# Performance work log

Measured on AMD Instinct MI355X. Metric: run time of the kernel, lower is better.

Reference implementation:

```python
import jax, jax.numpy as jnp
import numpy as np

NUM_ITER = 20
EPS = 1e-8


def _conv(x, w, pad):
    # x: [N, Cin, H, W], w: [Cout, Cin, kh, kw] (cross-correlation, like torch conv2d)
    return jax.lax.conv_general_dilated(
        x, w, window_strides=(1, 1), padding=pad,
        dimension_numbers=('NCHW', 'OIHW', 'NCHW'))


def setup_inputs() -> dict:
    key = jax.random.key(0)
    x = jax.random.normal(key, (2, 4, 3, 256, 256), dtype=jnp.float32)
    return {
        'x': x,
        'lam': jnp.array([0.02], dtype=jnp.float32),
        'tau': jnp.array([0.25], dtype=jnp.float32),
        'theta': jnp.array([0.1], dtype=jnp.float32),
        'wx': jnp.array([[-1.0, 1.0, 0.0]], dtype=jnp.float32),
        'wy': jnp.array([[-1.0], [1.0], [0.0]], dtype=jnp.float32),
    }


def reference(x, lam, tau, theta, wx, wy):
    # x: [2, B, C, H, W] -> pairs of single-channel images [NB, 2, H, W]
    F, B, C, H, W = x.shape
    NB = B * C
    xx = jnp.moveaxis(x.reshape(2, NB, H, W), 0, 1)  # [NB, 2, H, W]

    dt = x.dtype
    gx = jnp.array([[-1., 0., 1.], [-2., 0., 2.], [-1., 0., 1.]], dt) / 6.0
    gy = jnp.array([[-1., -2., -1.], [0., 0., 0.], [1., 2., 1.]], dt) / 6.0
    grad_w = jnp.stack([gx, gy])[:, None]          # [2,1,3,3] image gradient (fixed)
    gxu = jnp.array([[0., 0., 0.], [0., -1., 1.], [0., 0., 0.]], dt)
    gyu = jnp.array([[0., 0., 0.], [0., -1., 0.], [0., 1., 0.]], dt)
    grad_u_w = jnp.stack([gxu, gyu])[:, None]      # [2,1,3,3] flow gradient (fixed)
    wx_k = wx[None, None]                          # [1,1,1,3] trainable divergence stencil
    wy_k = wy[None, None]                          # [1,1,3,1]

    rho_c = (xx[:, 1] - xx[:, 0])[:, None]                       # [NB,1,H,W]
    grad_im = _conv(xx[:, 1:], grad_w, [(1, 1), (1, 1)])         # [NB,2,H,W]
    norm_grad = jnp.sum(grad_im * grad_im, axis=1, keepdims=True) + EPS

    u = jnp.zeros((NB, 2, H, W), dt)
    p1 = jnp.zeros((NB, 2, H, W), dt)
    p2 = jnp.zeros((NB, 2, H, W), dt)

    tl = theta * lam       # [1]
    tt = tau / theta       # [1]

    def div(p):  # p: [NB,2,H,W] -> [NB,1,H,W]
        return (_conv(p[:, 0:1], wx_k, [(0, 0), (1, 1)]) +
                _conv(p[:, 1:2], wy_k, [(1, 1), (0, 0)]))

    def body(carry, _):
        u, p1, p2 = carry
        rho = rho_c + jnp.sum(grad_im * u, axis=1, keepdims=True)
        th = tl * norm_grad
        v = u - jnp.where(jnp.abs(rho) < th,
                          rho * grad_im / norm_grad,
                          tl * grad_im * jnp.sign(rho))
        u0 = v[:, 0] + theta * div(p1)[:, 0]
        u1 = v[:, 1] + theta * div(p2)[:, 0]
        u = jnp.stack([u0, u1], axis=1)
        g1 = _conv(u[:, 0:1], grad_u_w, [(1, 1), (1, 1)])
        g2 = _conv(u[:, 1:2], grad_u_w, [(1, 1), (1, 1)])
        p1 = (p1 + tt * g1) / (1.0 + tt * jnp.sum(jnp.abs(g1), axis=1, keepdims=True))
        p2 = (p2 + tt * g2) / (1.0 + tt * jnp.sum(jnp.abs(g2), axis=1, keepdims=True))
        return (u, p1, p2), None

    (u, p1, p2), _ = jax.lax.scan(body, (u, p1, p2), None, length=NUM_ITER)
    return u.reshape(B, C, 2, H, W)
```

## Files before the change

kernel.cpp:

```cpp
#include <hip/hip_runtime.h>

#define W 256
#define H 256
#define HW (W*H)
#define NB 12
#define ROWS 16
#define BPI (H/ROWS)
#define NBLK (NB*BPI)
#define NTHREADS 1024
#define NUM_ITER 20
#define TVEPS 1e-8f
#define HPLANES 6
#define FLAG_MAGIC 0x5A170000


__device__ __forceinline__ float aload(const float* p) {
    return __hip_atomic_load(p, __ATOMIC_RELAXED, __HIP_MEMORY_SCOPE_AGENT);
}
__device__ __forceinline__ void astore(float* p, float v) {
    __hip_atomic_store(p, v, __ATOMIC_RELAXED, __HIP_MEMORY_SCOPE_AGENT);
}
__device__ __forceinline__ void waitflag(const int* f, int tgt) {
    while (__hip_atomic_load(f, __ATOMIC_RELAXED, __HIP_MEMORY_SCOPE_AGENT) != tgt)
        __builtin_amdgcn_s_sleep(1);
    asm volatile("" ::: "memory");
}
__device__ __forceinline__ void setflag(int* f, int tgt) {
    asm volatile("s_waitcnt vmcnt(0)" ::: "memory");
    __hip_atomic_store(f, tgt, __ATOMIC_RELAXED, __HIP_MEMORY_SCOPE_AGENT);
}
__device__ __forceinline__ float fastrcp(float x) { return __builtin_amdgcn_rcpf(x); }

#define LD4(dst, ptr) { const float4 _t = *reinterpret_cast<const float4*>(ptr); \
                        dst[0]=_t.x; dst[1]=_t.y; dst[2]=_t.z; dst[3]=_t.w; }
#define ST4(ptr, src) { float4 _t; _t.x=src[0]; _t.y=src[1]; _t.z=src[2]; _t.w=src[3]; \
                        *reinterpret_cast<float4*>(ptr) = _t; }

__global__ __launch_bounds__(NTHREADS, 1) void tvl1_uex_kernel(
    const float* __restrict__ xin,
    const float* __restrict__ lam,
    const float* __restrict__ tau,
    const float* __restrict__ theta,
    const float* __restrict__ wxv,
    const float* __restrict__ wyv,
    float* __restrict__ uout,
    float* __restrict__ halo,
    int* __restrict__ flags)
{
    __shared__ float xu0[ROWS][W];
    __shared__ float xu1[ROWS][W];
    __shared__ float xq1[ROWS][W];
    __shared__ float xq2[ROWS][W];

    const int tid  = threadIdx.x;
    const int lane = tid & 63;
    const int wv   = tid >> 6;
    const int x0   = lane << 2;
    const int b    = blockIdx.x;
    const int n    = b / BPI, bi = b % BPI;
    const int r0   = bi * ROWS;
    const int grow = r0 + wv;
    const bool notTop = (bi > 0), notBot = (bi < BPI-1);

    const float th0 = theta[0];
    const float tl  = th0 * lam[0];
    const float tt  = tau[0] / th0;
    const float wx0 = wxv[0], wx1 = wxv[1], wx2 = wxv[2];
    const float wy0 = wyv[0], wy1 = wyv[1], wy2 = wyv[2];

    const float* __restrict__ I0 = xin + (size_t)n * HW;
    const float* __restrict__ I1 = xin + (size_t)(NB + n) * HW;

    float rho[4], gxr[4], gyr[4];
    {
        #pragma unroll
        for (int c = 0; c < 4; ++c) {
            const int xc = x0 + c;
            const int idx = grow * W + xc;
            const bool xm = xc > 0, xp = xc < W-1, ym = grow > 0, yp = grow < H-1;
            float a00=0.f,a01=0.f,a02=0.f,a10=0.f,a12=0.f,a20=0.f,a21=0.f,a22=0.f;
            if (ym) { a01=I1[idx-W]; if (xm) a00=I1[idx-W-1]; if (xp) a02=I1[idx-W+1]; }
            if (xm) a10=I1[idx-1];
            if (xp) a12=I1[idx+1];
            if (yp) { a21=I1[idx+W]; if (xm) a20=I1[idx+W-1]; if (xp) a22=I1[idx+W+1]; }
            gxr[c] = ((a02-a00) + 2.f*(a12-a10) + (a22-a20)) * (1.f/6.f);
            gyr[c] = ((a20-a00) + 2.f*(a21-a01) + (a22-a02)) * (1.f/6.f);
            rho[c] = I1[idx] - I0[idx];
        }
    }

    for (int k = tid; k < ROWS*W; k += NTHREADS) {
        (&xu0[0][0])[k]=0.f; (&xu1[0][0])[k]=0.f;
        (&xq1[0][0])[k]=0.f; (&xq2[0][0])[k]=0.f;
    }
    float u0[4]={0,0,0,0}, u1[4]={0,0,0,0};
    float p1x[4]={0,0,0,0}, p1y[4]={0,0,0,0}, p2x[4]={0,0,0,0}, p2y[4]={0,0,0,0};
    __syncthreads();

    for (int it = 0; it < NUM_ITER; ++it) {
        const bool last = (it == NUM_ITER-1);

        float hym1[4]={0,0,0,0}, hym2[4]={0,0,0,0};
        float hyp1[4]={0,0,0,0}, hyp2[4]={0,0,0,0};
        if (it > 0) {
            int* fb = flags + (size_t)(it-1) * 3 * NBLK;
            const int tgt = FLAG_MAGIC | (it-1);
            if (wv == 0 && notTop) {
                if (lane == 0) waitflag(&fb[1*NBLK + (b-1)], tgt);
                const float* hu = halo + ((size_t)(it-1)*NBLK + (b-1)) * HPLANES * W;
                #pragma unroll
                for (int c = 0; c < 4; ++c) {
                    hym1[c] = aload(hu + 2*W + x0 + c);
                    hym2[c] = aload(hu + 3*W + x0 + c);
                }
            }
            if (wv == 15 && notBot) {
                if (lane == 0) waitflag(&fb[0*NBLK + (b+1)], tgt);
                const float* hd = halo + ((size_t)(it-1)*NBLK + (b+1)) * HPLANES * W;
                #pragma unroll
                for (int c = 0; c < 4; ++c) {
                    hyp1[c] = aload(hd + 0*W + x0 + c);
                    hyp2[c] = aload(hd + 1*W + x0 + c);
                }
            }
        }

        float pym1[4], pym2[4], pyp1[4], pyp2[4];
        if (wv > 0) { LD4(pym1, &xq1[wv-1][x0]); LD4(pym2, &xq2[wv-1][x0]); }
        else        { for (int c=0;c<4;++c){ pym1[c]=hym1[c]; pym2[c]=hym2[c]; } }
        if (wv < ROWS-1) { LD4(pyp1, &xq1[wv+1][x0]); LD4(pyp2, &xq2[wv+1][x0]); }
        else             { for (int c=0;c<4;++c){ pyp1[c]=hyp1[c]; pyp2[c]=hyp2[c]; } }

        float l1 = __shfl_up(p1x[3], 1);   float l2 = __shfl_up(p2x[3], 1);
        if (lane == 0) { l1 = 0.f; l2 = 0.f; }
        float r1 = __shfl_down(p1x[0], 1); float r2 = __shfl_down(p2x[0], 1);
        if (lane == 63) { r1 = 0.f; r2 = 0.f; }
        const float p1xm[4] = { l1, p1x[0], p1x[1], p1x[2] };
        const float p1xp[4] = { p1x[1], p1x[2], p1x[3], r1 };
        const float p2xm[4] = { l2, p2x[0], p2x[1], p2x[2] };
        const float p2xp[4] = { p2x[1], p2x[2], p2x[3], r2 };

        #pragma unroll
        for (int c = 0; c < 4; ++c) {
            const float r  = rho[c] + gxr[c]*u0[c] + gyr[c]*u1[c];
            const float ng = gxr[c]*gxr[c] + gyr[c]*gyr[c] + TVEPS;
            const float th = tl * ng;
            const float f  = (fabsf(r) < th) ? (r * fastrcp(ng)) : copysignf(tl, r);
            const float d1 = wx0*p1xm[c] + wx1*p1x[c] + wx2*p1xp[c]
                           + wy0*pym1[c] + wy1*p1y[c] + wy2*pyp1[c];
            const float d2 = wx0*p2xm[c] + wx1*p2x[c] + wx2*p2xp[c]
                           + wy0*pym2[c] + wy1*p2y[c] + wy2*pyp2[c];
            u0[c] = (u0[c] - f*gxr[c]) + th0*d1;
            u1[c] = (u1[c] - f*gyr[c]) + th0*d2;
        }

        if (last) {
            float* __restrict__ o0 = uout + (size_t)(2*n)   * HW + (size_t)grow * W + x0;
            float* __restrict__ o1 = uout + (size_t)(2*n+1) * HW + (size_t)grow * W + x0;
            ST4(o0, u0); ST4(o1, u1);
            break;
        }

        float* hwp = halo + ((size_t)it * NBLK + b) * HPLANES * W;
        int* fw = flags + (size_t)it * 3 * NBLK;
        const int ftgt = FLAG_MAGIC | it;
        if (wv == 0 && notTop) {
            #pragma unroll
            for (int c = 0; c < 4; ++c) {
                astore(hwp + 4*W + x0 + c, u0[c]);
                astore(hwp + 5*W + x0 + c, u1[c]);
            }
            if (lane == 0) setflag(&fw[2*NBLK + b], ftgt);
        }
        ST4(&xu0[wv][x0], u0); ST4(&xu1[wv][x0], u1);
        __syncthreads();

        float uy0[4], uy1[4];
        if (wv < ROWS-1) { LD4(uy0, &xu0[wv+1][x0]); LD4(uy1, &xu1[wv+1][x0]); }
        else if (grow == H-1) { for (int c=0;c<4;++c){ uy0[c]=0.f; uy1[c]=0.f; } }
        else {
            if (lane == 0) waitflag(&fw[2*NBLK + (b+1)], ftgt);
            const float* hd = halo + ((size_t)it*NBLK + (b+1)) * HPLANES * W;
            #pragma unroll
            for (int c = 0; c < 4; ++c) {
                uy0[c] = aload(hd + 4*W + x0 + c);
                uy1[c] = aload(hd + 5*W + x0 + c);
            }
        }
        float ur0 = __shfl_down(u0[0], 1), ur1 = __shfl_down(u1[0], 1);
        if (lane == 63) { ur0 = 0.f; ur1 = 0.f; }
        #pragma unroll
        for (int c = 0; c < 4; ++c) {
            const float uxp0 = (c < 3) ? u0[c+1] : ur0;
            const float uxp1 = (c < 3) ? u1[c+1] : ur1;
            const float g1x = uxp0 - u0[c];
            const float g1y = uy0[c] - u0[c];
            const float g2x = uxp1 - u1[c];
            const float g2y = uy1[c] - u1[c];
            const float rc1 = fastrcp(1.f + tt * (fabsf(g1x) + fabsf(g1y)));
            const float rc2 = fastrcp(1.f + tt * (fabsf(g2x) + fabsf(g2y)));
            p1x[c] = (p1x[c] + tt*g1x) * rc1;
            p1y[c] = (p1y[c] + tt*g1y) * rc1;
            p2x[c] = (p2x[c] + tt*g2x) * rc2;
            p2y[c] = (p2y[c] + tt*g2y) * rc2;
        }
        ST4(&xq1[wv][x0], p1y); ST4(&xq2[wv][x0], p2y);

        if (wv == 0 && notTop) {
            #pragma unroll
            for (int c = 0; c < 4; ++c) {
                astore(hwp + 0*W + x0 + c, p1y[c]);
                astore(hwp + 1*W + x0 + c, p2y[c]);
            }
            if (lane == 0) setflag(&fw[0*NBLK + b], ftgt);
        } else if (wv == ROWS-1 && notBot) {
            #pragma unroll
            for (int c = 0; c < 4; ++c) {
                astore(hwp + 2*W + x0 + c, p1y[c]);
                astore(hwp + 3*W + x0 + c, p2y[c]);
            }
            if (lane == 0) setflag(&fw[1*NBLK + b], ftgt);
        }
        __syncthreads();
    }
}


__global__ void precompute_kernel(const float* __restrict__ x,
                                  float* __restrict__ u,
                                  float* __restrict__ ws) {
    const int row = blockIdx.x;
    const int n = row / H, y = row % H;
    const int xx = threadIdx.x;
    const int idx = y * W + xx;
    const float* __restrict__ I0 = x + (size_t)n * HW;
    const float* __restrict__ I1 = x + (size_t)(NB + n) * HW;
    float* __restrict__ p1  = ws;
    float* __restrict__ p2  = ws + (size_t)2 * NB * HW;
    float* __restrict__ rho = ws + (size_t)4 * NB * HW;
    float* __restrict__ gxp = ws + (size_t)5 * NB * HW;
    float* __restrict__ gyp = ws + (size_t)6 * NB * HW;
    const float i1c = I1[idx];
    const bool xm = xx > 0, xp = xx < W - 1, ym = y > 0, yp = y < H - 1;
    float a00=0.f,a01=0.f,a02=0.f,a10=0.f,a12=0.f,a20=0.f,a21=0.f,a22=0.f;
    if (ym) { a01 = I1[idx-W]; if (xm) a00 = I1[idx-W-1]; if (xp) a02 = I1[idx-W+1]; }
    if (xm) a10 = I1[idx-1];
    if (xp) a12 = I1[idx+1];
    if (yp) { a21 = I1[idx+W]; if (xm) a20 = I1[idx+W-1]; if (xp) a22 = I1[idx+W+1]; }
    const float gxv = ((a02-a00) + 2.f*(a12-a10) + (a22-a20)) * (1.f/6.f);
    const float gyv = ((a20-a00) + 2.f*(a21-a01) + (a22-a02)) * (1.f/6.f);
    const size_t np = (size_t)n * HW;
    rho[np+idx] = i1c - I0[idx];
    gxp[np+idx] = gxv;
    gyp[np+idx] = gyv;
    u[(size_t)(2*n)*HW + idx] = 0.f;   u[(size_t)(2*n+1)*HW + idx] = 0.f;
    p1[(size_t)(2*n)*HW + idx] = 0.f;  p1[(size_t)(2*n+1)*HW + idx] = 0.f;
    p2[(size_t)(2*n)*HW + idx] = 0.f;  p2[(size_t)(2*n+1)*HW + idx] = 0.f;
}

__global__ void u_kernel(const float* __restrict__ ws,
                         float* __restrict__ u,
                         const float* __restrict__ lam,
                         const float* __restrict__ theta,
                         const float* __restrict__ wxv,
                         const float* __restrict__ wyv) {
    const int row = blockIdx.x;
    const int n = row / H, y = row % H;
    const int xx = threadIdx.x;
    const int idx = y * W + xx;
    const size_t np = (size_t)n * HW;
    const float* __restrict__ p1  = ws;
    const float* __restrict__ p2  = ws + (size_t)2 * NB * HW;
    const float* __restrict__ rho_c = ws + (size_t)4 * NB * HW;
    const float* __restrict__ gxp = ws + (size_t)5 * NB * HW;
    const float* __restrict__ gyp = ws + (size_t)6 * NB * HW;
    const float th0 = theta[0];
    const float tl = th0 * lam[0];
    const float wx0 = wxv[0], wx1 = wxv[1], wx2 = wxv[2];
    const float wy0 = wyv[0], wy1 = wyv[1], wy2 = wyv[2];
    const float gx = gxp[np+idx];
    const float gy = gyp[np+idx];
    float* __restrict__ u0p = u + (size_t)(2*n)*HW;
    float* __restrict__ u1p = u + (size_t)(2*n+1)*HW;
    const float u0 = u0p[idx], u1 = u1p[idx];
    const float rho = rho_c[np+idx] + gx*u0 + gy*u1;
    const float ng = gx*gx + gy*gy + TVEPS;
    const float th = tl * ng;
    float s0, s1;
    if (fabsf(rho) < th) { const float d = rho/ng; s0 = d*gx; s1 = d*gy; }
    else { const float sg = (rho > 0.f) ? 1.f : ((rho < 0.f) ? -1.f : 0.f);
           s0 = tl*gx*sg; s1 = tl*gy*sg; }
    const float v0 = u0 - s0, v1 = u1 - s1;
    const float* __restrict__ p1x = p1 + (size_t)(2*n)*HW;
    const float* __restrict__ p1y = p1 + (size_t)(2*n+1)*HW;
    const float* __restrict__ p2x = p2 + (size_t)(2*n)*HW;
    const float* __restrict__ p2y = p2 + (size_t)(2*n+1)*HW;
    float d1 = wx1*p1x[idx] + wy1*p1y[idx];
    float d2 = wx1*p2x[idx] + wy1*p2y[idx];
    if (xx > 0)     { d1 += wx0*p1x[idx-1]; d2 += wx0*p2x[idx-1]; }
    if (xx < W-1)   { d1 += wx2*p1x[idx+1]; d2 += wx2*p2x[idx+1]; }
    if (y > 0)      { d1 += wy0*p1y[idx-W]; d2 += wy0*p2y[idx-W]; }
    if (y < H-1)    { d1 += wy2*p1y[idx+W]; d2 += wy2*p2y[idx+W]; }
    u0p[idx] = v0 + th0*d1;
    u1p[idx] = v1 + th0*d2;
}

__global__ void p_kernel(const float* __restrict__ u,
                         float* __restrict__ ws,
                         const float* __restrict__ tau,
                         const float* __restrict__ theta) {
    const int row = blockIdx.x;
    const int n = row / H, y = row % H;
    const int xx = threadIdx.x;
    const int idx = y * W + xx;
    float* __restrict__ p1 = ws;
    float* __restrict__ p2 = ws + (size_t)2 * NB * HW;
    const float tt = tau[0] / theta[0];
    const float* __restrict__ u0p = u + (size_t)(2*n)*HW;
    const float* __restrict__ u1p = u + (size_t)(2*n+1)*HW;
    const float c0 = u0p[idx];
    const float g1x = ((xx < W-1) ? u0p[idx+1] : 0.f) - c0;
    const float g1y = ((y < H-1) ? u0p[idx+W] : 0.f) - c0;
    const float c1 = u1p[idx];
    const float g2x = ((xx < W-1) ? u1p[idx+1] : 0.f) - c1;
    const float g2y = ((y < H-1) ? u1p[idx+W] : 0.f) - c1;
    float* __restrict__ p1x = p1 + (size_t)(2*n)*HW;
    float* __restrict__ p1y = p1 + (size_t)(2*n+1)*HW;
    float* __restrict__ p2x = p2 + (size_t)(2*n)*HW;
    float* __restrict__ p2y = p2 + (size_t)(2*n+1)*HW;
    const float den1 = 1.f + tt * (fabsf(g1x) + fabsf(g1y));
    p1x[idx] = (p1x[idx] + tt*g1x) / den1;
    p1y[idx] = (p1y[idx] + tt*g1y) / den1;
    const float den2 = 1.f + tt * (fabsf(g2x) + fabsf(g2y));
    p2x[idx] = (p2x[idx] + tt*g2x) / den2;
    p2y[idx] = (p2y[idx] + tt*g2y) / den2;
}

extern "C" void kernel_launch(void* const* d_in, const int* in_sizes, int n_in,
                              void* d_out, int out_size, void* d_ws, size_t ws_size,
                              hipStream_t stream) {
    const float* x     = (const float*)d_in[0];
    const float* lam   = (const float*)d_in[1];
    const float* tau   = (const float*)d_in[2];
    const float* theta = (const float*)d_in[3];
    const float* wxv   = (const float*)d_in[4];
    const float* wyv   = (const float*)d_in[5];
    float* u = (float*)d_out;

    const size_t halo_floats = (size_t)(NUM_ITER-1) * NBLK * HPLANES * W;
    const size_t need = halo_floats * sizeof(float)
                      + (size_t)(NUM_ITER-1) * 3 * NBLK * sizeof(int);

    if (ws_size >= need) {
        float* halo = (float*)d_ws;
        int* flags = (int*)((char*)d_ws + halo_floats * sizeof(float));
        void* args[] = { (void*)&x, (void*)&lam, (void*)&tau, (void*)&theta,
                         (void*)&wxv, (void*)&wyv, (void*)&u, (void*)&halo, (void*)&flags };
        hipLaunchCooperativeKernel((void*)tvl1_uex_kernel, dim3(NBLK), dim3(NTHREADS),
                                   args, 0, stream);
    } else {
        float* ws = (float*)d_ws;
        const dim3 grid(NB * H);
        const dim3 block(W);
        precompute_kernel<<<grid, block, 0, stream>>>(x, u, ws);
        for (int it = 0; it < NUM_ITER; ++it) {
            u_kernel<<<grid, block, 0, stream>>>(ws, u, lam, theta, wxv, wyv);
            p_kernel<<<grid, block, 0, stream>>>(u, ws, tau, theta);
        }
    }
}
```

Baseline: 102.4 us.

## Recompute neighbor halo row locally to remove mid-iteration cross-block wait

Replaces the per-iteration exchange of u halo rows with redundant recomputation: the bottom wave computes the u update for the next block's first row itself, using p values that neighbor publishes in the previous iteration. Edge waves also compute their u update before waiting on halo flags and add the halo contribution afterward, so the flag wait overlaps with compute. This removes one inter-block flag wait per iteration at the cost of extra halo planes, extra global stores and loads, and duplicated arithmetic on one wave.

```diff
diff --git a/kernel.cpp b/kernel.cpp
--- a/kernel.cpp
+++ b/kernel.cpp
@@ -10,7 +10,7 @@
 #define NTHREADS 1024
 #define NUM_ITER 20
 #define TVEPS 1e-8f
-#define HPLANES 6
+#define HPLANES 8
 #define FLAG_MAGIC 0x5A170000
 
 
@@ -35,8 +35,9 @@
                         dst[0]=_t.x; dst[1]=_t.y; dst[2]=_t.z; dst[3]=_t.w; }
 #define ST4(ptr, src) { float4 _t; _t.x=src[0]; _t.y=src[1]; _t.z=src[2]; _t.w=src[3]; \
                         *reinterpret_cast<float4*>(ptr) = _t; }
-
-__global__ __launch_bounds__(NTHREADS, 1) void tvl1_uex_kernel(
+#define CP4(dst, src) { _Pragma("unroll") for (int c = 0; c < 4; ++c) dst[c] = src[c]; }
+
+__global__ __launch_bounds__(NTHREADS, 1) void tvl1_dfr_kernel(
     const float* __restrict__ xin,
     const float* __restrict__ lam,
     const float* __restrict__ tau,
@@ -71,23 +72,28 @@
     const float* __restrict__ I0 = xin + (size_t)n * HW;
     const float* __restrict__ I1 = xin + (size_t)(NB + n) * HW;
 
-    float rho[4], gxr[4], gyr[4];
-    {
+    auto grad4 = [&](int row, float* rr, float* ggx, float* ggy) {
         #pragma unroll
         for (int c = 0; c < 4; ++c) {
             const int xc = x0 + c;
-            const int idx = grow * W + xc;
-            const bool xm = xc > 0, xp = xc < W-1, ym = grow > 0, yp = grow < H-1;
+            const int idx = row * W + xc;
+            const bool xm = xc > 0, xp = xc < W-1, ym = row > 0, yp = row < H-1;
             float a00=0.f,a01=0.f,a02=0.f,a10=0.f,a12=0.f,a20=0.f,a21=0.f,a22=0.f;
             if (ym) { a01=I1[idx-W]; if (xm) a00=I1[idx-W-1]; if (xp) a02=I1[idx-W+1]; }
             if (xm) a10=I1[idx-1];
             if (xp) a12=I1[idx+1];
             if (yp) { a21=I1[idx+W]; if (xm) a20=I1[idx+W-1]; if (xp) a22=I1[idx+W+1]; }
-            gxr[c] = ((a02-a00) + 2.f*(a12-a10) + (a22-a20)) * (1.f/6.f);
-            gyr[c] = ((a20-a00) + 2.f*(a21-a01) + (a22-a02)) * (1.f/6.f);
-            rho[c] = I1[idx] - I0[idx];
-        }
-    }
+            ggx[c] = ((a02-a00) + 2.f*(a12-a10) + (a22-a20)) * (1.f/6.f);
+            ggy[c] = ((a20-a00) + 2.f*(a21-a01) + (a22-a02)) * (1.f/6.f);
+            rr[c]  = I1[idx] - I0[idx];
+        }
+    };
+
+    float rho[4], gxr[4], gyr[4];
+    grad4(grow, rho, gxr, gyr);
+    float rho16[4]={0,0,0,0}, gx16[4]={0,0,0,0}, gy16[4]={0,0,0,0};
+    float u16_0[4]={0,0,0,0}, u16_1[4]={0,0,0,0};
+    if (wv == 15 && notBot) grad4(r0 + ROWS, rho16, gx16, gy16);
 
     for (int k = tid; k < ROWS*W; k += NTHREADS) {
         (&xu0[0][0])[k]=0.f; (&xu1[0][0])[k]=0.f;
@@ -97,61 +103,147 @@
     float p1x[4]={0,0,0,0}, p1y[4]={0,0,0,0}, p2x[4]={0,0,0,0}, p2y[4]={0,0,0,0};
     __syncthreads();
 
-    for (int it = 0; it < NUM_ITER; ++it) {
-        const bool last = (it == NUM_ITER-1);
-
-        float hym1[4]={0,0,0,0}, hym2[4]={0,0,0,0};
-        float hyp1[4]={0,0,0,0}, hyp2[4]={0,0,0,0};
-        if (it > 0) {
-            int* fb = flags + (size_t)(it-1) * 3 * NBLK;
-            const int tgt = FLAG_MAGIC | (it-1);
-            if (wv == 0 && notTop) {
-                if (lane == 0) waitflag(&fb[1*NBLK + (b-1)], tgt);
-                const float* hu = halo + ((size_t)(it-1)*NBLK + (b-1)) * HPLANES * W;
-                #pragma unroll
-                for (int c = 0; c < 4; ++c) {
-                    hym1[c] = aload(hu + 2*W + x0 + c);
-                    hym2[c] = aload(hu + 3*W + x0 + c);
-                }
-            }
-            if (wv == 15 && notBot) {
-                if (lane == 0) waitflag(&fb[0*NBLK + (b+1)], tgt);
-                const float* hd = halo + ((size_t)(it-1)*NBLK + (b+1)) * HPLANES * W;
-                #pragma unroll
-                for (int c = 0; c < 4; ++c) {
-                    hyp1[c] = aload(hd + 0*W + x0 + c);
-                    hyp2[c] = aload(hd + 1*W + x0 + c);
-                }
-            }
-        }
-
-        float pym1[4], pym2[4], pyp1[4], pyp2[4];
-        if (wv > 0) { LD4(pym1, &xq1[wv-1][x0]); LD4(pym2, &xq2[wv-1][x0]); }
-        else        { for (int c=0;c<4;++c){ pym1[c]=hym1[c]; pym2[c]=hym2[c]; } }
-        if (wv < ROWS-1) { LD4(pyp1, &xq1[wv+1][x0]); LD4(pyp2, &xq2[wv+1][x0]); }
-        else             { for (int c=0;c<4;++c){ pyp1[c]=hyp1[c]; pyp2[c]=hyp2[c]; } }
-
-        float l1 = __shfl_up(p1x[3], 1);   float l2 = __shfl_up(p2x[3], 1);
+    auto ustep_dym = [&](const float* rr, const float* ggx, const float* ggy,
+                         const float* uu0, const float* uu1,
+                         const float* x1, const float* q1c, const float* q1p,
+                         const float* x2, const float* q2c, const float* q2p,
+                         float* o0, float* o1) {
+        float l1 = __shfl_up(x1[3],1), l2 = __shfl_up(x2[3],1);
         if (lane == 0) { l1 = 0.f; l2 = 0.f; }
-        float r1 = __shfl_down(p1x[0], 1); float r2 = __shfl_down(p2x[0], 1);
+        float r1 = __shfl_down(x1[0],1), r2 = __shfl_down(x2[0],1);
         if (lane == 63) { r1 = 0.f; r2 = 0.f; }
-        const float p1xm[4] = { l1, p1x[0], p1x[1], p1x[2] };
-        const float p1xp[4] = { p1x[1], p1x[2], p1x[3], r1 };
-        const float p2xm[4] = { l2, p2x[0], p2x[1], p2x[2] };
-        const float p2xp[4] = { p2x[1], p2x[2], p2x[3], r2 };
-
+        const float x1m[4]={l1,x1[0],x1[1],x1[2]}, x1p[4]={x1[1],x1[2],x1[3],r1};
+        const float x2m[4]={l2,x2[0],x2[1],x2[2]}, x2p[4]={x2[1],x2[2],x2[3],r2};
+        #pragma unroll
+        for (int c = 0; c < 4; ++c) {
+            const float r  = rr[c] + ggx[c]*uu0[c] + ggy[c]*uu1[c];
+            const float ng = ggx[c]*ggx[c] + ggy[c]*ggy[c] + TVEPS;
+            const float f  = (fabsf(r) < tl*ng) ? (r * fastrcp(ng)) : copysignf(tl, r);
+            const float d1 = wx0*x1m[c] + wx1*x1[c] + wx2*x1p[c] + wy1*q1c[c] + wy2*q1p[c];
+            const float d2 = wx0*x2m[c] + wx1*x2[c] + wx2*x2p[c] + wy1*q2c[c] + wy2*q2p[c];
+            o0[c] = (uu0[c] - f*ggx[c]) + th0*d1;
+            o1[c] = (uu1[c] - f*ggy[c]) + th0*d2;
+        }
+    };
+    auto ustep_dyp = [&](const float* rr, const float* ggx, const float* ggy,
+                         const float* uu0, const float* uu1,
+                         const float* x1, const float* q1m, const float* q1c,
+                         const float* x2, const float* q2m, const float* q2c,
+                         float* o0, float* o1) {
+        float l1 = __shfl_up(x1[3],1), l2 = __shfl_up(x2[3],1);
+        if (lane == 0) { l1 = 0.f; l2 = 0.f; }
+        float r1 = __shfl_down(x1[0],1), r2 = __shfl_down(x2[0],1);
+        if (lane == 63) { r1 = 0.f; r2 = 0.f; }
+        const float x1m[4]={l1,x1[0],x1[1],x1[2]}, x1p[4]={x1[1],x1[2],x1[3],r1};
+        const float x2m[4]={l2,x2[0],x2[1],x2[2]}, x2p[4]={x2[1],x2[2],x2[3],r2};
+        #pragma unroll
+        for (int c = 0; c < 4; ++c) {
+            const float r  = rr[c] + ggx[c]*uu0[c] + ggy[c]*uu1[c];
+            const float ng = ggx[c]*ggx[c] + ggy[c]*ggy[c] + TVEPS;
+            const float f  = (fabsf(r) < tl*ng) ? (r * fastrcp(ng)) : copysignf(tl, r);
+            const float d1 = wx0*x1m[c] + wx1*x1[c] + wx2*x1p[c] + wy0*q1m[c] + wy1*q1c[c];
+            const float d2 = wx0*x2m[c] + wx1*x2[c] + wx2*x2p[c] + wy0*q2m[c] + wy1*q2c[c];
+            o0[c] = (uu0[c] - f*ggx[c]) + th0*d1;
+            o1[c] = (uu1[c] - f*ggy[c]) + th0*d2;
+        }
+    };
+    auto ustepF = [&](const float* q1m, const float* q1p, const float* q2m, const float* q2p) {
+        float l1 = __shfl_up(p1x[3],1), l2 = __shfl_up(p2x[3],1);
+        if (lane == 0) { l1 = 0.f; l2 = 0.f; }
+        float r1 = __shfl_down(p1x[0],1), r2 = __shfl_down(p2x[0],1);
+        if (lane == 63) { r1 = 0.f; r2 = 0.f; }
+        const float x1m[4]={l1,p1x[0],p1x[1],p1x[2]}, x1p[4]={p1x[1],p1x[2],p1x[3],r1};
+        const float x2m[4]={l2,p2x[0],p2x[1],p2x[2]}, x2p[4]={p2x[1],p2x[2],p2x[3],r2};
         #pragma unroll
         for (int c = 0; c < 4; ++c) {
             const float r  = rho[c] + gxr[c]*u0[c] + gyr[c]*u1[c];
             const float ng = gxr[c]*gxr[c] + gyr[c]*gyr[c] + TVEPS;
-            const float th = tl * ng;
-            const float f  = (fabsf(r) < th) ? (r * fastrcp(ng)) : copysignf(tl, r);
-            const float d1 = wx0*p1xm[c] + wx1*p1x[c] + wx2*p1xp[c]
-                           + wy0*pym1[c] + wy1*p1y[c] + wy2*pyp1[c];
-            const float d2 = wx0*p2xm[c] + wx1*p2x[c] + wx2*p2xp[c]
-                           + wy0*pym2[c] + wy1*p2y[c] + wy2*pyp2[c];
+            const float f  = (fabsf(r) < tl*ng) ? (r * fastrcp(ng)) : copysignf(tl, r);
+            const float d1 = wx0*x1m[c] + wx1*p1x[c] + wx2*x1p[c]
+                           + wy0*q1m[c] + wy1*p1y[c] + wy2*q1p[c];
+            const float d2 = wx0*x2m[c] + wx1*p2x[c] + wx2*x2p[c]
+                           + wy0*q2m[c] + wy1*p2y[c] + wy2*q2p[c];
             u0[c] = (u0[c] - f*gxr[c]) + th0*d1;
             u1[c] = (u1[c] - f*gyr[c]) + th0*d2;
+        }
+    };
+
+    for (int it = 0; it < NUM_ITER; ++it) {
+        const bool last = (it == NUM_ITER-1);
+
+        if (wv == 0) {
+            float pyp1[4], pyp2[4];
+            LD4(pyp1, &xq1[1][x0]); LD4(pyp2, &xq2[1][x0]);
+            float o0[4], o1[4];
+            ustep_dym(rho, gxr, gyr, u0, u1, p1x, p1y, pyp1, p2x, p2y, pyp2, o0, o1);
+            float hym1[4]={0,0,0,0}, hym2[4]={0,0,0,0};
+            if (it > 0 && notTop) {
+                int* fb = flags + (size_t)(it-1)*3*NBLK;
+                if (lane == 0) waitflag(&fb[2*NBLK + (b-1)], FLAG_MAGIC | (it-1));
+                const float* hp = halo + ((size_t)(it-1)*NBLK + (b-1))*HPLANES*W;
+                #pragma unroll
+                for (int c = 0; c < 4; ++c) {
+                    hym1[c] = aload(hp + 6*W + x0 + c);
+                    hym2[c] = aload(hp + 7*W + x0 + c);
+                }
+            }
+            #pragma unroll
+            for (int c = 0; c < 4; ++c) {
+                u0[c] = o0[c] + th0*(wy0*hym1[c]);
+                u1[c] = o1[c] + th0*(wy0*hym2[c]);
+            }
+        } else if (wv == 15) {
+            float pym1[4], pym2[4];
+            LD4(pym1, &xq1[14][x0]); LD4(pym2, &xq2[14][x0]);
+            float o0[4], o1[4];
+            ustep_dyp(rho, gxr, gyr, u0, u1, p1x, pym1, p1y, p2x, pym2, p2y, o0, o1);
+            float hyp1[4]={0,0,0,0}, hyp2[4]={0,0,0,0};
+            float cx1[4]={0,0,0,0}, cx2[4]={0,0,0,0};
+            float cp1[4]={0,0,0,0}, cp2[4]={0,0,0,0};
+            if (it > 0 && notBot) {
+                int* fb = flags + (size_t)(it-1)*3*NBLK;
+                const int nw = last ? 1 : 2;
+                if (lane < nw) waitflag(&fb[lane*NBLK + (b+1)], FLAG_MAGIC | (it-1));
+                const float* hp = halo + ((size_t)(it-1)*NBLK + (b+1))*HPLANES*W;
+                #pragma unroll
+                for (int c = 0; c < 4; ++c) {
+                    hyp1[c] = aload(hp + 1*W + x0 + c);
+                    hyp2[c] = aload(hp + 3*W + x0 + c);
+                }
+                if (!last) {
+                    #pragma unroll
+                    for (int c = 0; c < 4; ++c) {
+                        cx1[c] = aload(hp + 0*W + x0 + c);
+                        cx2[c] = aload(hp + 2*W + x0 + c);
+                        cp1[c] = aload(hp + 4*W + x0 + c);
+                        cp2[c] = aload(hp + 5*W + x0 + c);
+                    }
+                }
+            }
+            #pragma unroll
+            for (int c = 0; c < 4; ++c) {
+                u0[c] = o0[c] + th0*(wy2*hyp1[c]);
+                u1[c] = o1[c] + th0*(wy2*hyp2[c]);
+            }
+            if (!last) {
+                ST4(&xu0[15][x0], u0); ST4(&xu1[15][x0], u1);
+                if (notBot) {
+                    float o160[4], o161[4];
+                    ustep_dym(rho16, gx16, gy16, u16_0, u16_1,
+                              cx1, hyp1, cp1, cx2, hyp2, cp2, o160, o161);
+                    #pragma unroll
+                    for (int c = 0; c < 4; ++c) {
+                        u16_0[c] = o160[c] + th0*(wy0*p1y[c]);
+                        u16_1[c] = o161[c] + th0*(wy0*p2y[c]);
+                    }
+                }
+            }
+        } else {
+            float pym1[4], pym2[4], pyp1[4], pyp2[4];
+            LD4(pym1, &xq1[wv-1][x0]); LD4(pym2, &xq2[wv-1][x0]);
+            LD4(pyp1, &xq1[wv+1][x0]); LD4(pyp2, &xq2[wv+1][x0]);
+            ustepF(pym1, pyp1, pym2, pyp2);
+            ST4(&xu0[wv][x0], u0); ST4(&xu1[wv][x0], u1);
         }
 
         if (last) {
@@ -160,33 +252,12 @@
             ST4(o0, u0); ST4(o1, u1);
             break;
         }
-
-        float* hwp = halo + ((size_t)it * NBLK + b) * HPLANES * W;
-        int* fw = flags + (size_t)it * 3 * NBLK;
-        const int ftgt = FLAG_MAGIC | it;
-        if (wv == 0 && notTop) {
-            #pragma unroll
-            for (int c = 0; c < 4; ++c) {
-                astore(hwp + 4*W + x0 + c, u0[c]);
-                astore(hwp + 5*W + x0 + c, u1[c]);
-            }
-            if (lane == 0) setflag(&fw[2*NBLK + b], ftgt);
-        }
-        ST4(&xu0[wv][x0], u0); ST4(&xu1[wv][x0], u1);
         __syncthreads();
 
         float uy0[4], uy1[4];
-        if (wv < ROWS-1) { LD4(uy0, &xu0[wv+1][x0]); LD4(uy1, &xu1[wv+1][x0]); }
-        else if (grow == H-1) { for (int c=0;c<4;++c){ uy0[c]=0.f; uy1[c]=0.f; } }
-        else {
-            if (lane == 0) waitflag(&fw[2*NBLK + (b+1)], ftgt);
-            const float* hd = halo + ((size_t)it*NBLK + (b+1)) * HPLANES * W;
-            #pragma unroll
-            for (int c = 0; c < 4; ++c) {
-                uy0[c] = aload(hd + 4*W + x0 + c);
-                uy1[c] = aload(hd + 5*W + x0 + c);
-            }
-        }
+        if (wv < 15)            { LD4(uy0, &xu0[wv+1][x0]); LD4(uy1, &xu1[wv+1][x0]); }
+        else if (grow == H-1)   { for (int c=0;c<4;++c){ uy0[c]=0.f; uy1[c]=0.f; } }
+        else                    { CP4(uy0, u16_0); CP4(uy1, u16_1); }
         float ur0 = __shfl_down(u0[0], 1), ur1 = __shfl_down(u1[0], 1);
         if (lane == 63) { ur0 = 0.f; ur1 = 0.f; }
         #pragma unroll
@@ -206,20 +277,34 @@
         }
         ST4(&xq1[wv][x0], p1y); ST4(&xq2[wv][x0], p2y);
 
-        if (wv == 0 && notTop) {
-            #pragma unroll
-            for (int c = 0; c < 4; ++c) {
-                astore(hwp + 0*W + x0 + c, p1y[c]);
-                astore(hwp + 1*W + x0 + c, p2y[c]);
-            }
-            if (lane == 0) setflag(&fw[0*NBLK + b], ftgt);
-        } else if (wv == ROWS-1 && notBot) {
-            #pragma unroll
-            for (int c = 0; c < 4; ++c) {
-                astore(hwp + 2*W + x0 + c, p1y[c]);
-                astore(hwp + 3*W + x0 + c, p2y[c]);
-            }
-            if (lane == 0) setflag(&fw[1*NBLK + b], ftgt);
+        {
+            float* hw = halo + ((size_t)it * NBLK + b) * HPLANES * W;
+            int* fw = flags + (size_t)it * 3 * NBLK;
+            const int ft = FLAG_MAGIC | it;
+            if (wv == 0 && notTop) {
+                #pragma unroll
+                for (int c = 0; c < 4; ++c) {
+                    astore(hw + 0*W + x0 + c, p1x[c]);
+                    astore(hw + 1*W + x0 + c, p1y[c]);
+                    astore(hw + 2*W + x0 + c, p2x[c]);
+                    astore(hw + 3*W + x0 + c, p2y[c]);
+                }
+                if (lane == 0) setflag(&fw[0*NBLK + b], ft);
+            } else if (wv == 1 && notTop) {
+                #pragma unroll
+                for (int c = 0; c < 4; ++c) {
+                    astore(hw + 4*W + x0 + c, p1y[c]);
+                    astore(hw + 5*W + x0 + c, p2y[c]);
+                }
+                if (lane == 0) setflag(&fw[1*NBLK + b], ft);
+            } else if (wv == 15 && notBot) {
+                #pragma unroll
+                for (int c = 0; c < 4; ++c) {
+                    astore(hw + 6*W + x0 + c, p1y[c]);
+                    astore(hw + 7*W + x0 + c, p2y[c]);
+                }
+                if (lane == 0) setflag(&fw[2*NBLK + b], ft);
+            }
         }
         __syncthreads();
     }
@@ -291,16 +376,16 @@
     else { const float sg = (rho > 0.f) ? 1.f : ((rho < 0.f) ? -1.f : 0.f);
            s0 = tl*gx*sg; s1 = tl*gy*sg; }
     const float v0 = u0 - s0, v1 = u1 - s1;
-    const float* __restrict__ p1x = p1 + (size_t)(2*n)*HW;
-    const float* __restrict__ p1y = p1 + (size_t)(2*n+1)*HW;
-    const float* __restrict__ p2x = p2 + (size_t)(2*n)*HW;
-    const float* __restrict__ p2y = p2 + (size_t)(2*n+1)*HW;
-    float d1 = wx1*p1x[idx] + wy1*p1y[idx];
-    float d2 = wx1*p2x[idx] + wy1*p2y[idx];
-    if (xx > 0)     { d1 += wx0*p1x[idx-1]; d2 += wx0*p2x[idx-1]; }
-    if (xx < W-1)   { d1 += wx2*p1x[idx+1]; d2 += wx2*p2x[idx+1]; }
-    if (y > 0)      { d1 += wy0*p1y[idx-W]; d2 += wy0*p2y[idx-W]; }
-    if (y < H-1)    { d1 += wy2*p1y[idx+W]; d2 += wy2*p2y[idx+W]; }
+    const float* __restrict__ p1xp = p1 + (size_t)(2*n)*HW;
+    const float* __restrict__ p1yp = p1 + (size_t)(2*n+1)*HW;
+    const float* __restrict__ p2xp = p2 + (size_t)(2*n)*HW;
+    const float* __restrict__ p2yp = p2 + (size_t)(2*n+1)*HW;
+    float d1 = wx1*p1xp[idx] + wy1*p1yp[idx];
+    float d2 = wx1*p2xp[idx] + wy1*p2yp[idx];
+    if (xx > 0)     { d1 += wx0*p1xp[idx-1]; d2 += wx0*p2xp[idx-1]; }
+    if (xx < W-1)   { d1 += wx2*p1xp[idx+1]; d2 += wx2*p2xp[idx+1]; }
+    if (y > 0)      { d1 += wy0*p1yp[idx-W]; d2 += wy0*p2yp[idx-W]; }
+    if (y < H-1)    { d1 += wy2*p1yp[idx+W]; d2 += wy2*p2yp[idx+W]; }
     u0p[idx] = v0 + th0*d1;
     u1p[idx] = v1 + th0*d2;
 }
@@ -324,16 +409,16 @@
     const float c1 = u1p[idx];
     const float g2x = ((xx < W-1) ? u1p[idx+1] : 0.f) - c1;
     const float g2y = ((y < H-1) ? u1p[idx+W] : 0.f) - c1;
-    float* __restrict__ p1x = p1 + (size_t)(2*n)*HW;
-    float* __restrict__ p1y = p1 + (size_t)(2*n+1)*HW;
-    float* __restrict__ p2x = p2 + (size_t)(2*n)*HW;
-    float* __restrict__ p2y = p2 + (size_t)(2*n+1)*HW;
+    float* __restrict__ p1xp = p1 + (size_t)(2*n)*HW;
+    float* __restrict__ p1yp = p1 + (size_t)(2*n+1)*HW;
+    float* __restrict__ p2xp = p2 + (size_t)(2*n)*HW;
+    float* __restrict__ p2yp = p2 + (size_t)(2*n+1)*HW;
     const float den1 = 1.f + tt * (fabsf(g1x) + fabsf(g1y));
-    p1x[idx] = (p1x[idx] + tt*g1x) / den1;
-    p1y[idx] = (p1y[idx] + tt*g1y) / den1;
+    p1xp[idx] = (p1xp[idx] + tt*g1x) / den1;
+    p1yp[idx] = (p1yp[idx] + tt*g1y) / den1;
     const float den2 = 1.f + tt * (fabsf(g2x) + fabsf(g2y));
-    p2x[idx] = (p2x[idx] + tt*g2x) / den2;
-    p2y[idx] = (p2y[idx] + tt*g2y) / den2;
+    p2xp[idx] = (p2xp[idx] + tt*g2x) / den2;
+    p2yp[idx] = (p2yp[idx] + tt*g2y) / den2;
 }
 
 extern "C" void kernel_launch(void* const* d_in, const int* in_sizes, int n_in,
@@ -356,7 +441,7 @@
         int* flags = (int*)((char*)d_ws + halo_floats * sizeof(float));
         void* args[] = { (void*)&x, (void*)&lam, (void*)&tau, (void*)&theta,
                          (void*)&wxv, (void*)&wyv, (void*)&u, (void*)&halo, (void*)&flags };
-        hipLaunchCooperativeKernel((void*)tvl1_uex_kernel, dim3(NBLK), dim3(NTHREADS),
+        hipLaunchCooperativeKernel((void*)tvl1_dfr_kernel, dim3(NBLK), dim3(NTHREADS),
                                    args, 0, stream);
     } else {
         float* ws = (float*)d_ws;
```

Result: slower. 123.3 us (+20.4%).
